# Optimization experiments

Hardware: AMD Instinct MI355X
Metric: run time of the kernel (lower is better)

Reference implementation:

```python
import jax, jax.numpy as jnp
import numpy as np

NUM_STEPS = 32
SEQ = 64
IN = 512
HID = 256
NUM_CLASSES = 10
BATCH = 2048


def _lstm_layer(xseq, Wih, Whh, bih, bhh):
    # xseq: (T, B, D). PyTorch LSTMCell gate order: i, f, g, o.
    B = xseq.shape[1]
    H = Whh.shape[1]
    h0 = jnp.zeros((B, H), xseq.dtype)
    c0 = jnp.zeros((B, H), xseq.dtype)
    b = bih + bhh

    def step(carry, x):
        h, c = carry
        gates = x @ Wih.T + h @ Whh.T + b  # (B, 4H)
        i, f, g, o = jnp.split(gates, 4, axis=-1)
        c_new = jax.nn.sigmoid(f) * c + jax.nn.sigmoid(i) * jnp.tanh(g)
        h_new = jax.nn.sigmoid(o) * jnp.tanh(c_new)
        return (h_new, c_new), h_new

    (hT, cT), hs = jax.lax.scan(step, (h0, c0), xseq)
    return hs, hT


def _run_stack(xseq, layer_params):
    hT = None
    for (Wih, Whh, bih, bhh) in layer_params:
        xseq, hT = _lstm_layer(xseq, Wih, Whh, bih, bhh)
    return hT


def setup_inputs() -> dict:
    key = jax.random.key(0)
    ks = jax.random.split(key, 32)
    d = {"xs": jax.random.normal(ks[0], (BATCH, SEQ, IN), dtype=jnp.float32)}
    cfg = [IN, HID, HID]
    ki = 1
    for direc in ("f", "r"):
        for l, (di, dh) in enumerate(zip(cfg[:-1], cfg[1:])):
            s = 1.0 / np.sqrt(dh)
            d[f"Wih_{direc}{l}"] = jax.random.uniform(ks[ki], (4 * dh, di), minval=-s, maxval=s); ki += 1
            d[f"Whh_{direc}{l}"] = jax.random.uniform(ks[ki], (4 * dh, dh), minval=-s, maxval=s); ki += 1
            d[f"bih_{direc}{l}"] = jax.random.uniform(ks[ki], (4 * dh,), minval=-s, maxval=s); ki += 1
            d[f"bhh_{direc}{l}"] = jax.random.uniform(ks[ki], (4 * dh,), minval=-s, maxval=s); ki += 1
    s = 1.0 / np.sqrt(2 * HID)
    d["W3"] = jax.random.uniform(ks[ki], (NUM_CLASSES, 2 * HID), minval=-s, maxval=s); ki += 1
    d["b3"] = jax.random.uniform(ks[ki], (NUM_CLASSES,), minval=-s, maxval=s)
    return d


def reference(xs, Wih_f0, Whh_f0, bih_f0, bhh_f0, Wih_f1, Whh_f1, bih_f1, bhh_f1,
              Wih_r0, Whh_r0, bih_r0, bhh_r0, Wih_r1, Whh_r1, bih_r1, bhh_r1, W3, b3):
    # forward direction: timesteps 62-NUM_STEPS .. 61
    xf = jnp.transpose(xs[:, 62 - NUM_STEPS:62, :], (1, 0, 2))  # (T, B, D)
    hF = _run_stack(xf, [(Wih_f0, Whh_f0, bih_f0, bhh_f0),
                         (Wih_f1, Whh_f1, bih_f1, bhh_f1)])
    # reverse direction: last 3 frames in order 63, 62, 61
    xr = jnp.transpose(jnp.flip(xs[:, 61:64, :], axis=1), (1, 0, 2))  # (3, B, D)
    hR = _run_stack(xr, [(Wih_r0, Whh_r0, bih_r0, bhh_r0),
                         (Wih_r1, Whh_r1, bih_r1, bhh_r1)])
    latent = jnp.concatenate([hF, hR], axis=1)  # (B, 512)
    return latent @ W3.T + b3
```

## Files before the change

kernel.cpp:

```cpp
#include <hip/hip_runtime.h>
#include <stdint.h>

typedef unsigned short u16;
typedef unsigned long long u64;
typedef __attribute__((ext_vector_type(8)))  short  bf16x8;
typedef __attribute__((ext_vector_type(8)))  u16    u16x8;
typedef __attribute__((ext_vector_type(4)))  float  f32x4;
typedef __attribute__((ext_vector_type(16))) _Float16 f16x16;

#define MFMA_BF16(a,b,c) __builtin_amdgcn_mfma_f32_16x16x32_bf16((a),(b),(c),0,0,0)

#define BATCH   2048
#define FSTEPS  32
#define RSTEPS  3
#define NVF     35

static constexpr size_t HROW32 = 128;
static constexpr size_t HPAR32 = (size_t)BATCH * HROW32;

static constexpr size_t OFF_CTL  = 0;
static constexpr size_t OFF_H0G  = 32768;
static constexpr size_t OFF_H1G  = OFF_H0G + HPAR32 * 2 * 4;
static constexpr size_t OFF_LAT  = OFF_H1G + HPAR32 * 2 * 4;
static constexpr size_t OFF_XP   = OFF_LAT + (size_t)BATCH * 512 * 4;
static constexpr size_t XP_BYTES = (size_t)NVF * BATCH * 1024 * 2;
static constexpr size_t OFF_W0XF = OFF_XP + XP_BYTES;
static constexpr size_t OFF_W0XR = OFF_W0XF + (size_t)1024 * 512 * 2;
static constexpr size_t OFF_P0F  = OFF_W0XR + (size_t)1024 * 512 * 2;
static constexpr size_t OFF_P0R  = OFF_P0F + (size_t)32768 * 16;
static constexpr size_t OFF_P1F  = OFF_P0R + (size_t)32768 * 16;
static constexpr size_t OFF_P1R  = OFF_P1F + (size_t)65536 * 16;
static constexpr size_t OFF_BS0F = OFF_P1R + (size_t)65536 * 16;
static constexpr size_t OFF_BS0R = OFF_BS0F + 4096;
static constexpr size_t OFF_BS1F = OFF_BS0R + 4096;
static constexpr size_t OFF_BS1R = OFF_BS1F + 4096;
static constexpr size_t WS_NEED  = OFF_BS1R + 4096;

__device__ __forceinline__ u16 f2bf(float f) {
    unsigned u = __float_as_uint(f);
    unsigned r = (u + 0x7fffu + ((u >> 16) & 1u)) >> 16;
    return (u16)r;
}
__device__ __forceinline__ float sigm(float x) { return 1.0f / (1.0f + __expf(-x)); }
__device__ __forceinline__ float tanh_fast(float x) {
    float a = fabsf(x);
    float e = __expf(-2.0f * a);
    float t = (1.0f - e) / (1.0f + e);
    return x < 0.0f ? -t : t;
}

__device__ __forceinline__ bf16x8 ldsA(const char* H, int row, int k) {
    int byte = (row << 9) + (k << 1);
    byte ^= (row & 7) << 4;
    return *(const bf16x8*)(H + byte);
}

__device__ __forceinline__ void reload32(char* Hs, const u64* src, int rg, int tid) {
    u64 v[8];
#pragma unroll
    for (int i = 0; i < 8; ++i) {
        int idx = tid + (i << 8);
        v[i] = __hip_atomic_load(src + ((size_t)rg * 32 + (idx >> 6)) * 64 + (idx & 63),
                                 __ATOMIC_RELAXED, __HIP_MEMORY_SCOPE_AGENT);
    }
#pragma unroll
    for (int i = 0; i < 8; ++i) {
        int idx = tid + (i << 8);
        int row = idx >> 6, cu = idx & 63;
        int byte = (row << 9) + (cu << 3);
        byte ^= (row & 7) << 4;
        *(u64*)(Hs + byte) = v[i];
    }
}

__global__ void __launch_bounds__(256)
lstm_seq(const _Float16* __restrict__ xp,
         const u16* __restrict__ P0f_, const u16* __restrict__ P0r_,
         const u16* __restrict__ P1f_, const u16* __restrict__ P1r_,
         const float* __restrict__ bs1f, const float* __restrict__ bs1r,
         unsigned* __restrict__ h0g, unsigned* __restrict__ h1g,
         float* __restrict__ latent, unsigned* __restrict__ ctl)
{
    __shared__ char T0[16384];
    __shared__ char T1[16384];
    const int tid = threadIdx.x, wq = tid >> 6, lane = tid & 63;
    const int bid = blockIdx.x;
    const int colq = bid >> 6;
    const int rg   = bid & 63;
    const int mem  = colq * 4 + wq;
    const int hc   = mem * 16 + (lane & 15);
    const int klane = lane >> 4, q4 = klane << 2;
    unsigned* flag = ctl + (size_t)rg * 64;
    unsigned bcount = 0;

    for (int dir = 0; dir < 2; ++dir) {
        const int nst = dir ? RSTEPS : FSTEPS;
        const int gbase = dir ? FSTEPS : 0;
        const bf16x8* P0v = (const bf16x8*)(dir ? P0r_ : P0f_) + (size_t)mem * (8 * 4 * 64);
        const bf16x8* P1v = (const bf16x8*)(dir ? P1r_ : P1f_) + (size_t)mem * (16 * 4 * 64);
        const float* bs1 = dir ? bs1r : bs1f;
        float b1reg[4];
#pragma unroll
        for (int g = 0; g < 4; ++g) b1reg[g] = bs1[g * 256 + hc];

        float c0[2][4], c1[2][4];
#pragma unroll
        for (int Mt = 0; Mt < 2; ++Mt)
#pragma unroll
            for (int r = 0; r < 4; ++r) { c0[Mt][r] = 0.f; c1[Mt][r] = 0.f; }

        __syncthreads();
#pragma unroll
        for (int i = 0; i < 4; ++i) {
            ((f32x4*)T0)[i * 256 + tid] = (f32x4){0.f, 0.f, 0.f, 0.f};
            ((f32x4*)T1)[i * 256 + tid] = (f32x4){0.f, 0.f, 0.f, 0.f};
        }
        __syncthreads();

        f16x16 xqm[2];
#pragma unroll
        for (int Mt = 0; Mt < 2; ++Mt)
            xqm[Mt] = *(const f16x16*)(xp +
                ((((size_t)gbase * 128 + rg * 2 + Mt) * 16 + mem) * 64 + lane) * 16);

        for (int t = 0; t <= nst; ++t) {
            f32x4 acc1[4][2];
            if (t >= 1) {
#pragma unroll
                for (int g = 0; g < 4; ++g) { acc1[g][0] = (f32x4){0.f,0.f,0.f,0.f}; acc1[g][1] = (f32x4){0.f,0.f,0.f,0.f}; }
#pragma unroll
                for (int kc = 0; kc < 8; ++kc) {
                    bf16x8 a0 = ldsA(T0, (lane & 15),       kc * 32 + klane * 8);
                    bf16x8 a1 = ldsA(T0, 16 + (lane & 15),  kc * 32 + klane * 8);
#pragma unroll
                    for (int g = 0; g < 4; ++g) {
                        bf16x8 b = P1v[(kc * 4 + g) * 64 + lane];
                        acc1[g][0] = MFMA_BF16(a0, b, acc1[g][0]);
                        acc1[g][1] = MFMA_BF16(a1, b, acc1[g][1]);
                    }
                }
                if (t >= 2) {
#pragma unroll
                    for (int kc = 0; kc < 8; ++kc) {
                        bf16x8 a0 = ldsA(T1, (lane & 15),      kc * 32 + klane * 8);
                        bf16x8 a1 = ldsA(T1, 16 + (lane & 15), kc * 32 + klane * 8);
#pragma unroll
                        for (int g = 0; g < 4; ++g) {
                            bf16x8 b = P1v[((kc + 8) * 4 + g) * 64 + lane];
                            acc1[g][0] = MFMA_BF16(a0, b, acc1[g][0]);
                            acc1[g][1] = MFMA_BF16(a1, b, acc1[g][1]);
                        }
                    }
                }
            }

            f32x4 acc0[4][2];
            if (t < nst) {
#pragma unroll
                for (int g = 0; g < 4; ++g) { acc0[g][0] = (f32x4){0.f,0.f,0.f,0.f}; acc0[g][1] = (f32x4){0.f,0.f,0.f,0.f}; }
                if (t >= 1) {
#pragma unroll
                    for (int kc = 0; kc < 8; ++kc) {
                        bf16x8 a0 = ldsA(T0, (lane & 15),      kc * 32 + klane * 8);
                        bf16x8 a1 = ldsA(T0, 16 + (lane & 15), kc * 32 + klane * 8);
#pragma unroll
                        for (int g = 0; g < 4; ++g) {
                            bf16x8 b = P0v[(kc * 4 + g) * 64 + lane];
                            acc0[g][0] = MFMA_BF16(a0, b, acc0[g][0]);
                            acc0[g][1] = MFMA_BF16(a1, b, acc0[g][1]);
                        }
                    }
                }
            }

            if (t < nst) {
                unsigned* dst = h0g + (size_t)(t & 1) * HPAR32;
                const int cp = mem * 8 + ((lane & 15) >> 1);
#pragma unroll
                for (int Mt = 0; Mt < 2; ++Mt) {
                    float hn[4];
#pragma unroll
                    for (int r = 0; r < 4; ++r) {
                        float gi = acc0[0][Mt][r] + (float)xqm[Mt][0 * 4 + r];
                        float gf = acc0[1][Mt][r] + (float)xqm[Mt][1 * 4 + r];
                        float gg = acc0[2][Mt][r] + (float)xqm[Mt][2 * 4 + r];
                        float go = acc0[3][Mt][r] + (float)xqm[Mt][3 * 4 + r];
                        float cn = sigm(gf) * c0[Mt][r] + sigm(gi) * tanh_fast(gg);
                        c0[Mt][r] = cn;
                        hn[r] = sigm(go) * tanh_fast(cn);
                    }
                    const int rowbase = rg * 32 + Mt * 16 + q4;
#pragma unroll
                    for (int r = 0; r < 4; ++r) {
                        float p = __shfl_xor(hn[r], 1);
                        if (!(lane & 1)) {
                            unsigned w = (unsigned)f2bf(hn[r]) | ((unsigned)f2bf(p) << 16);
                            __hip_atomic_store(dst + (size_t)(rowbase + r) * HROW32 + cp, w,
                                               __ATOMIC_RELAXED, __HIP_MEMORY_SCOPE_AGENT);
                        }
                    }
                }
            }

            if (t >= 1) {
                const int cp = mem * 8 + ((lane & 15) >> 1);
#pragma unroll
                for (int Mt = 0; Mt < 2; ++Mt) {
                    float hn[4];
#pragma unroll
                    for (int r = 0; r < 4; ++r) {
                        float gi = acc1[0][Mt][r] + b1reg[0];
                        float gf = acc1[1][Mt][r] + b1reg[1];
                        float gg = acc1[2][Mt][r] + b1reg[2];
                        float go = acc1[3][Mt][r] + b1reg[3];
                        float cn = sigm(gf) * c1[Mt][r] + sigm(gi) * tanh_fast(gg);
                        c1[Mt][r] = cn;
                        hn[r] = sigm(go) * tanh_fast(cn);
                    }
                    const int rowbase = rg * 32 + Mt * 16 + q4;
                    if (t < nst) {
                        unsigned* dst = h1g + (size_t)((t - 1) & 1) * HPAR32;
#pragma unroll
                        for (int r = 0; r < 4; ++r) {
                            float p = __shfl_xor(hn[r], 1);
                            if (!(lane & 1)) {
                                unsigned w = (unsigned)f2bf(hn[r]) | ((unsigned)f2bf(p) << 16);
                                __hip_atomic_store(dst + (size_t)(rowbase + r) * HROW32 + cp, w,
                                                   __ATOMIC_RELAXED, __HIP_MEMORY_SCOPE_AGENT);
                            }
                        }
                    } else {
#pragma unroll
                        for (int r = 0; r < 4; ++r)
                            latent[(size_t)(rowbase + r) * 512 + dir * 256 + hc] = hn[r];
                    }
                }
            }

            if (t < nst) {
                ++bcount;
                asm volatile("s_waitcnt vmcnt(0)" ::: "memory");
                __syncthreads();
                if (tid == 0)
                    __hip_atomic_fetch_add(flag, 1u, __ATOMIC_RELAXED, __HIP_MEMORY_SCOPE_AGENT);
                if (t + 1 < nst) {
#pragma unroll
                    for (int Mt = 0; Mt < 2; ++Mt)
                        xqm[Mt] = *(const f16x16*)(xp +
                            ((((size_t)(gbase + t + 1) * 128 + rg * 2 + Mt) * 16 + mem) * 64 + lane) * 16);
                }
                if (tid == 0) {
                    while (__hip_atomic_load(flag, __ATOMIC_RELAXED, __HIP_MEMORY_SCOPE_AGENT)
                           < 4u * bcount) {}
                }
                __syncthreads();
                __builtin_amdgcn_sched_barrier(0);
                reload32(T0, (const u64*)(h0g + (size_t)(t & 1) * HPAR32), rg, tid);
                if (t >= 1)
                    reload32(T1, (const u64*)(h1g + (size_t)((t - 1) & 1) * HPAR32), rg, tid);
                __syncthreads();
            }
        }
    }
}

__global__ void __launch_bounds__(256)
xproj_gemm(const float* __restrict__ xs,
           const u16* __restrict__ W0xf, const u16* __restrict__ W0xr,
           const float* __restrict__ bs0f, const float* __restrict__ bs0r,
           _Float16* __restrict__ xp)
{
    __shared__ char As[16384];
    __shared__ char Bs[16384];
    const int tid = threadIdx.x, wv = tid >> 6, lane = tid & 63;
    const int phys = blockIdx.x;
    const int xcd = phys & 7, idx = phys >> 3;
    const int mt = xcd * 70 + (idx >> 3);
    const int nt = idx & 7;
    const int vf = mt >> 4;
    const int dirr = (vf >= 32);
    const int frame = dirr ? (95 - vf) : (30 + vf);
    const int brow = (mt & 15) * 128;
    const u16* Wp = (dirr ? W0xr : W0xf) + (size_t)nt * 128 * 512;
    const float* bs = dirr ? bs0r : bs0f;

    float breg[8];
#pragma unroll
    for (int n = 0; n < 8; ++n) breg[n] = bs[nt * 128 + n * 16 + (lane & 15)];

    f32x4 acc[8][2];
#pragma unroll
    for (int n = 0; n < 8; ++n) { acc[n][0] = (f32x4){0.f,0.f,0.f,0.f}; acc[n][1] = (f32x4){0.f,0.f,0.f,0.f}; }

    const int ar = tid >> 1, akoff = (tid & 1) * 32;
    const float* asrc0 = xs + ((size_t)(brow + ar) * 64 + frame) * 512 + akoff;

    for (int c = 0; c < 8; ++c) {
        {
            const float* s = asrc0 + c * 64;
            u16x8 o[4];
#pragma unroll
            for (int j2 = 0; j2 < 4; ++j2) {
                float4 f0 = *(const float4*)(s + j2 * 8);
                float4 f1 = *(const float4*)(s + j2 * 8 + 4);
                u16x8 o_;
                o_[0] = f2bf(f0.x); o_[1] = f2bf(f0.y); o_[2] = f2bf(f0.z); o_[3] = f2bf(f0.w);
                o_[4] = f2bf(f1.x); o_[5] = f2bf(f1.y); o_[6] = f2bf(f1.z); o_[7] = f2bf(f1.w);
                o[j2] = o_;
            }
#pragma unroll
            for (int j2 = 0; j2 < 4; ++j2) {
                int k = akoff + j2 * 8;
                int byte = (ar << 7) + (k << 1); byte ^= (ar & 7) << 4;
                *(u16x8*)(As + byte) = o[j2];
            }
        }
#pragma unroll
        for (int i = 0; i < 4; ++i) {
            int u = tid + i * 256;
            int ns = u >> 3, c8 = (u & 7) << 3;
            u16x8 v = *(const u16x8*)(Wp + (size_t)ns * 512 + c * 64 + c8);
            int byte = (ns << 7) + (c8 << 1); byte ^= (ns & 7) << 4;
            *(u16x8*)(Bs + byte) = v;
        }
        __syncthreads();
#pragma unroll
        for (int kk = 0; kk < 2; ++kk) {
            int kin = kk * 32 + (lane >> 4) * 8;
            bf16x8 a0, a1;
            int row = wv * 32 + (lane & 15);
            int byte = (row << 7) + (kin << 1); byte ^= (row & 7) << 4;
            a0 = *(const bf16x8*)(As + byte);
            int row1 = row + 16;
            byte = (row1 << 7) + (kin << 1); byte ^= (row1 & 7) << 4;
            a1 = *(const bf16x8*)(As + byte);
#pragma unroll
            for (int n = 0; n < 8; ++n) {
                int ns = n * 16 + (lane & 15);
                int bb = (ns << 7) + (kin << 1); bb ^= (ns & 7) << 4;
                bf16x8 bf_ = *(const bf16x8*)(Bs + bb);
                acc[n][0] = MFMA_BF16(a0, bf_, acc[n][0]);
                acc[n][1] = MFMA_BF16(a1, bf_, acc[n][1]);
            }
        }
        __syncthreads();
    }
#pragma unroll
    for (int n = 0; n < 8; ++n)
#pragma unroll
        for (int mm = 0; mm < 2; ++mm)
#pragma unroll
            for (int r = 0; r < 4; ++r) {
                int vm  = mt * 128 + wv * 32 + mm * 16 + ((lane >> 4) << 2) + r;
                int col = nt * 128 + n * 16 + (lane & 15);
                int vf2 = vm >> 11, brow2 = vm & 2047;
                int rb2 = brow2 >> 4, sub = brow2 & 15;
                int lane2 = ((sub >> 2) << 4) + (col & 15);
                int m2 = (col >> 4) & 15, g2 = col >> 8;
                size_t o = ((((size_t)vf2 * 128 + rb2) * 16 + m2) * 64 + lane2) * 16
                           + (g2 << 2) + (sub & 3);
                xp[o] = (_Float16)(acc[n][mm][r] + breg[n]);
            }
}

__global__ void pack_w(const float* __restrict__ Wa, int da,
                       const float* __restrict__ bi, const float* __restrict__ bh,
                       u16* __restrict__ Wout, float* __restrict__ bout)
{
    int total = 1024 * da;
    int gt = blockIdx.x * blockDim.x + threadIdx.x;
    int stride = gridDim.x * blockDim.x;
    for (int i = gt; i < total; i += stride) Wout[i] = f2bf(Wa[i]);
    if (bout && gt < 1024) bout[gt] = bi[gt] + bh[gt];
}

__global__ void pack_frag(const float* __restrict__ Wa, int da,
                          const float* __restrict__ Wb, int db,
                          int nkc, u16* __restrict__ out,
                          const float* __restrict__ bi, const float* __restrict__ bh,
                          float* __restrict__ bout)
{
    int total = 16 * nkc * 4 * 64;
    int gt = blockIdx.x * blockDim.x + threadIdx.x;
    int stride = gridDim.x * blockDim.x;
    for (int u = gt; u < total; u += stride) {
        int l = u & 63;
        int t1 = u >> 6;
        int g = t1 & 3;
        int t2 = t1 >> 2;
        int kc = t2 % nkc;
        int mem = t2 / nkc;
        int row = g * 256 + mem * 16 + (l & 15);
        int k0 = kc * 32 + ((l >> 4) << 3);
        u16x8 o;
#pragma unroll
        for (int jj = 0; jj < 8; ++jj) {
            int k = k0 + jj;
            float v = (k < da) ? Wa[(size_t)row * da + k] : Wb[(size_t)row * db + (k - da)];
            o[jj] = f2bf(v);
        }
        *(u16x8*)(out + (size_t)u * 8) = o;
    }
    if (bout && gt < 1024) bout[gt] = bi[gt] + bh[gt];
}

__global__ void final_linear(const float* __restrict__ latent, const float* __restrict__ W3,
                             const float* __restrict__ b3, float* __restrict__ out)
{
    int idx = blockIdx.x * blockDim.x + threadIdx.x;
    if (idx >= BATCH * 10) return;
    int bb = idx / 10, c = idx - bb * 10;
    const float* lrow = latent + (size_t)bb * 512;
    const float* wrow = W3 + (size_t)c * 512;
    float s = b3[c];
#pragma unroll 4
    for (int k = 0; k < 512; k += 4) {
        float4 lv = *(const float4*)(lrow + k);
        float4 wv = *(const float4*)(wrow + k);
        s += lv.x * wv.x + lv.y * wv.y + lv.z * wv.z + lv.w * wv.w;
    }
    out[idx] = s;
}

extern "C" void kernel_launch(void* const* d_in, const int* in_sizes, int n_in,
                              void* d_out, int out_size, void* d_ws, size_t ws_size,
                              hipStream_t stream)
{
    (void)in_sizes; (void)n_in; (void)out_size;
    if (ws_size < WS_NEED) return;

    const float* xs     = (const float*)d_in[0];
    const float* Wih_f0 = (const float*)d_in[1];
    const float* Whh_f0 = (const float*)d_in[2];
    const float* bih_f0 = (const float*)d_in[3];
    const float* bhh_f0 = (const float*)d_in[4];
    const float* Wih_f1 = (const float*)d_in[5];
    const float* Whh_f1 = (const float*)d_in[6];
    const float* bih_f1 = (const float*)d_in[7];
    const float* bhh_f1 = (const float*)d_in[8];
    const float* Wih_r0 = (const float*)d_in[9];
    const float* Whh_r0 = (const float*)d_in[10];
    const float* bih_r0 = (const float*)d_in[11];
    const float* bhh_r0 = (const float*)d_in[12];
    const float* Wih_r1 = (const float*)d_in[13];
    const float* Whh_r1 = (const float*)d_in[14];
    const float* bih_r1 = (const float*)d_in[15];
    const float* bhh_r1 = (const float*)d_in[16];
    const float* W3     = (const float*)d_in[17];
    const float* b3     = (const float*)d_in[18];

    char* ws = (char*)d_ws;
    unsigned* ctl = (unsigned*)(ws + OFF_CTL);
    unsigned* h0g = (unsigned*)(ws + OFF_H0G);
    unsigned* h1g = (unsigned*)(ws + OFF_H1G);
    float* latent = (float*)(ws + OFF_LAT);
    _Float16* xp  = (_Float16*)(ws + OFF_XP);
    u16* W0xf = (u16*)(ws + OFF_W0XF);
    u16* W0xr = (u16*)(ws + OFF_W0XR);
    u16* P0f  = (u16*)(ws + OFF_P0F);
    u16* P0r  = (u16*)(ws + OFF_P0R);
    u16* P1f  = (u16*)(ws + OFF_P1F);
    u16* P1r  = (u16*)(ws + OFF_P1R);
    float* bs0f = (float*)(ws + OFF_BS0F);
    float* bs0r = (float*)(ws + OFF_BS0R);
    float* bs1f = (float*)(ws + OFF_BS1F);
    float* bs1r = (float*)(ws + OFF_BS1R);

    hipMemsetAsync(ctl, 0, 32768, stream);

    pack_w<<<256, 256, 0, stream>>>(Wih_f0, 512, bih_f0, bhh_f0, W0xf, bs0f);
    pack_w<<<256, 256, 0, stream>>>(Wih_r0, 512, bih_r0, bhh_r0, W0xr, bs0r);
    pack_frag<<<64, 256, 0, stream>>>(Whh_f0, 256, Whh_f0, 0, 8,  P0f, nullptr, nullptr, nullptr);
    pack_frag<<<64, 256, 0, stream>>>(Whh_r0, 256, Whh_r0, 0, 8,  P0r, nullptr, nullptr, nullptr);
    pack_frag<<<64, 256, 0, stream>>>(Wih_f1, 256, Whh_f1, 256, 16, P1f, bih_f1, bhh_f1, bs1f);
    pack_frag<<<64, 256, 0, stream>>>(Wih_r1, 256, Whh_r1, 256, 16, P1r, bih_r1, bhh_r1, bs1r);

    xproj_gemm<<<4480, 256, 0, stream>>>(xs, W0xf, W0xr, bs0f, bs0r, xp);

    lstm_seq<<<256, 256, 0, stream>>>(xp, P0f, P0r, P1f, P1r, bs1f, bs1r,
                                      h0g, h1g, latent, ctl);

    final_linear<<<80, 256, 0, stream>>>(latent, W3, b3, (float*)d_out);
}
```

Before: 871.1 us.

## Split recurrent LSTM matmuls across two wave groups and pre-convert inputs to bf16

The persistent LSTM kernel now runs 512 threads per block. Two halves of the waves split the layer-0 and layer-1 recurrent K work, exchange partial accumulators through LDS, and each half applies one layer's gate nonlinearity. The aim is to shorten the serial per-step critical path by using more waves per CU. A separate pack_x kernel converts the needed input frames to bf16 once, so the projection GEMM can load bf16 directly instead of converting fp32 per tile. This adds an extra LDS round trip and sync per step, plus an extra pass over the input.

```diff
diff --git a/kernel.cpp b/kernel.cpp
--- a/kernel.cpp
+++ b/kernel.cpp
@@ -14,27 +14,10 @@
 #define FSTEPS  32
 #define RSTEPS  3
 #define NVF     35
+#define NXF     34
 
 static constexpr size_t HROW32 = 128;
 static constexpr size_t HPAR32 = (size_t)BATCH * HROW32;
-
-static constexpr size_t OFF_CTL  = 0;
-static constexpr size_t OFF_H0G  = 32768;
-static constexpr size_t OFF_H1G  = OFF_H0G + HPAR32 * 2 * 4;
-static constexpr size_t OFF_LAT  = OFF_H1G + HPAR32 * 2 * 4;
-static constexpr size_t OFF_XP   = OFF_LAT + (size_t)BATCH * 512 * 4;
-static constexpr size_t XP_BYTES = (size_t)NVF * BATCH * 1024 * 2;
-static constexpr size_t OFF_W0XF = OFF_XP + XP_BYTES;
-static constexpr size_t OFF_W0XR = OFF_W0XF + (size_t)1024 * 512 * 2;
-static constexpr size_t OFF_P0F  = OFF_W0XR + (size_t)1024 * 512 * 2;
-static constexpr size_t OFF_P0R  = OFF_P0F + (size_t)32768 * 16;
-static constexpr size_t OFF_P1F  = OFF_P0R + (size_t)32768 * 16;
-static constexpr size_t OFF_P1R  = OFF_P1F + (size_t)65536 * 16;
-static constexpr size_t OFF_BS0F = OFF_P1R + (size_t)65536 * 16;
-static constexpr size_t OFF_BS0R = OFF_BS0F + 4096;
-static constexpr size_t OFF_BS1F = OFF_BS0R + 4096;
-static constexpr size_t OFF_BS1R = OFF_BS1F + 4096;
-static constexpr size_t WS_NEED  = OFF_BS1R + 4096;
 
 __device__ __forceinline__ u16 f2bf(float f) {
     unsigned u = __float_as_uint(f);
@@ -55,17 +38,17 @@
     return *(const bf16x8*)(H + byte);
 }
 
-__device__ __forceinline__ void reload32(char* Hs, const u64* src, int rg, int tid) {
-    u64 v[8];
-#pragma unroll
-    for (int i = 0; i < 8; ++i) {
-        int idx = tid + (i << 8);
+__device__ __forceinline__ void reload512(char* Hs, const u64* src, int rg, int tid) {
+    u64 v[4];
+#pragma unroll
+    for (int i = 0; i < 4; ++i) {
+        int idx = tid + (i << 9);
         v[i] = __hip_atomic_load(src + ((size_t)rg * 32 + (idx >> 6)) * 64 + (idx & 63),
                                  __ATOMIC_RELAXED, __HIP_MEMORY_SCOPE_AGENT);
     }
 #pragma unroll
-    for (int i = 0; i < 8; ++i) {
-        int idx = tid + (i << 8);
+    for (int i = 0; i < 4; ++i) {
+        int idx = tid + (i << 9);
         int row = idx >> 6, cu = idx & 63;
         int byte = (row << 9) + (cu << 3);
         byte ^= (row & 7) << 4;
@@ -73,7 +56,7 @@
     }
 }
 
-__global__ void __launch_bounds__(256)
+__global__ void __launch_bounds__(512, 1)
 lstm_seq(const _Float16* __restrict__ xp,
          const u16* __restrict__ P0f_, const u16* __restrict__ P0r_,
          const u16* __restrict__ P1f_, const u16* __restrict__ P1r_,
@@ -81,15 +64,21 @@
          unsigned* __restrict__ h0g, unsigned* __restrict__ h1g,
          float* __restrict__ latent, unsigned* __restrict__ ctl)
 {
-    __shared__ char T0[16384];
-    __shared__ char T1[16384];
-    const int tid = threadIdx.x, wq = tid >> 6, lane = tid & 63;
+    extern __shared__ char lds[];
+    char* T0 = lds;
+    char* T1 = lds + 16384;
+    char* SA = lds + 32768;
+    char* SB = lds + 65536;
+
+    const int tid = threadIdx.x, w = tid >> 6, lane = tid & 63;
+    const int wq = w & 3, kh = w >> 2;
     const int bid = blockIdx.x;
     const int colq = bid >> 6;
     const int rg   = bid & 63;
     const int mem  = colq * 4 + wq;
     const int hc   = mem * 16 + (lane & 15);
     const int klane = lane >> 4, q4 = klane << 2;
+    const int sbase = (wq * 64 + lane) * 16;
     unsigned* flag = ctl + (size_t)rg * 64;
     unsigned bcount = 0;
 
@@ -111,34 +100,56 @@
 
         __syncthreads();
 #pragma unroll
-        for (int i = 0; i < 4; ++i) {
-            ((f32x4*)T0)[i * 256 + tid] = (f32x4){0.f, 0.f, 0.f, 0.f};
-            ((f32x4*)T1)[i * 256 + tid] = (f32x4){0.f, 0.f, 0.f, 0.f};
+        for (int i = 0; i < 4; ++i)
+            ((f32x4*)lds)[i * 512 + tid] = (f32x4){0.f, 0.f, 0.f, 0.f};
+        __syncthreads();
+
+        f16x16 xqm[2];
+        if (kh == 1) {
+#pragma unroll
+            for (int Mt = 0; Mt < 2; ++Mt)
+                xqm[Mt] = *(const f16x16*)(xp +
+                    ((((size_t)gbase * 128 + rg * 2 + Mt) * 16 + mem) * 64 + lane) * 16);
         }
-        __syncthreads();
-
-        f16x16 xqm[2];
-#pragma unroll
-        for (int Mt = 0; Mt < 2; ++Mt)
-            xqm[Mt] = *(const f16x16*)(xp +
-                ((((size_t)gbase * 128 + rg * 2 + Mt) * 16 + mem) * 64 + lane) * 16);
 
         for (int t = 0; t <= nst; ++t) {
-            f32x4 acc1[4][2];
-            if (t >= 1) {
-#pragma unroll
-                for (int g = 0; g < 4; ++g) { acc1[g][0] = (f32x4){0.f,0.f,0.f,0.f}; acc1[g][1] = (f32x4){0.f,0.f,0.f,0.f}; }
-#pragma unroll
-                for (int kc = 0; kc < 8; ++kc) {
-                    bf16x8 a0 = ldsA(T0, (lane & 15),       kc * 32 + klane * 8);
-                    bf16x8 a1 = ldsA(T0, 16 + (lane & 15),  kc * 32 + klane * 8);
-#pragma unroll
-                    for (int g = 0; g < 4; ++g) {
-                        bf16x8 b = P1v[(kc * 4 + g) * 64 + lane];
-                        acc1[g][0] = MFMA_BF16(a0, b, acc1[g][0]);
-                        acc1[g][1] = MFMA_BF16(a1, b, acc1[g][1]);
+            f32x4 acc1[4][2], acc0[4][2];
+#pragma unroll
+            for (int g = 0; g < 4; ++g)
+#pragma unroll
+                for (int Mt = 0; Mt < 2; ++Mt) {
+                    acc1[g][Mt] = (f32x4){0.f, 0.f, 0.f, 0.f};
+                    acc0[g][Mt] = (f32x4){0.f, 0.f, 0.f, 0.f};
+                }
+
+            if (kh == 0) {
+                if (t >= 1) {
+#pragma unroll
+                    for (int kc = 0; kc < 8; ++kc) {
+                        bf16x8 a0 = ldsA(T0, (lane & 15),      kc * 32 + klane * 8);
+                        bf16x8 a1 = ldsA(T0, 16 + (lane & 15), kc * 32 + klane * 8);
+#pragma unroll
+                        for (int g = 0; g < 4; ++g) {
+                            bf16x8 b = P1v[(kc * 4 + g) * 64 + lane];
+                            acc1[g][0] = MFMA_BF16(a0, b, acc1[g][0]);
+                            acc1[g][1] = MFMA_BF16(a1, b, acc1[g][1]);
+                        }
                     }
-                }
+                    if (t < nst) {
+#pragma unroll
+                        for (int kc = 0; kc < 4; ++kc) {
+                            bf16x8 a0 = ldsA(T0, (lane & 15),      kc * 32 + klane * 8);
+                            bf16x8 a1 = ldsA(T0, 16 + (lane & 15), kc * 32 + klane * 8);
+#pragma unroll
+                            for (int g = 0; g < 4; ++g) {
+                                bf16x8 b = P0v[(kc * 4 + g) * 64 + lane];
+                                acc0[g][0] = MFMA_BF16(a0, b, acc0[g][0]);
+                                acc0[g][1] = MFMA_BF16(a1, b, acc0[g][1]);
+                            }
+                        }
+                    }
+                }
+            } else {
                 if (t >= 2) {
 #pragma unroll
                     for (int kc = 0; kc < 8; ++kc) {
@@ -152,15 +163,9 @@
                         }
                     }
                 }
-            }
-
-            f32x4 acc0[4][2];
-            if (t < nst) {
-#pragma unroll
-                for (int g = 0; g < 4; ++g) { acc0[g][0] = (f32x4){0.f,0.f,0.f,0.f}; acc0[g][1] = (f32x4){0.f,0.f,0.f,0.f}; }
-                if (t >= 1) {
-#pragma unroll
-                    for (int kc = 0; kc < 8; ++kc) {
+                if (t >= 1 && t < nst) {
+#pragma unroll
+                    for (int kc = 4; kc < 8; ++kc) {
                         bf16x8 a0 = ldsA(T0, (lane & 15),      kc * 32 + klane * 8);
                         bf16x8 a1 = ldsA(T0, 16 + (lane & 15), kc * 32 + klane * 8);
 #pragma unroll
@@ -173,66 +178,89 @@
                 }
             }
 
-            if (t < nst) {
-                unsigned* dst = h0g + (size_t)(t & 1) * HPAR32;
-                const int cp = mem * 8 + ((lane & 15) >> 1);
-#pragma unroll
-                for (int Mt = 0; Mt < 2; ++Mt) {
-                    float hn[4];
-#pragma unroll
-                    for (int r = 0; r < 4; ++r) {
-                        float gi = acc0[0][Mt][r] + (float)xqm[Mt][0 * 4 + r];
-                        float gf = acc0[1][Mt][r] + (float)xqm[Mt][1 * 4 + r];
-                        float gg = acc0[2][Mt][r] + (float)xqm[Mt][2 * 4 + r];
-                        float go = acc0[3][Mt][r] + (float)xqm[Mt][3 * 4 + r];
-                        float cn = sigm(gf) * c0[Mt][r] + sigm(gi) * tanh_fast(gg);
-                        c0[Mt][r] = cn;
-                        hn[r] = sigm(go) * tanh_fast(cn);
+            {
+                char* S = kh ? SA : SB;
+#pragma unroll
+                for (int g = 0; g < 4; ++g)
+#pragma unroll
+                    for (int Mt = 0; Mt < 2; ++Mt)
+                        *(f32x4*)(S + (g * 2 + Mt) * 4096 + sbase) =
+                            kh ? acc1[g][Mt] : acc0[g][Mt];
+            }
+            __syncthreads();
+
+            if (kh == 0) {
+                if (t >= 1) {
+#pragma unroll
+                    for (int g = 0; g < 4; ++g)
+#pragma unroll
+                        for (int Mt = 0; Mt < 2; ++Mt)
+                            acc1[g][Mt] += *(const f32x4*)(SA + (g * 2 + Mt) * 4096 + sbase);
+                    const int cp = mem * 8 + ((lane & 15) >> 1);
+#pragma unroll
+                    for (int Mt = 0; Mt < 2; ++Mt) {
+                        float hn[4];
+#pragma unroll
+                        for (int r = 0; r < 4; ++r) {
+                            float gi = acc1[0][Mt][r] + b1reg[0];
+                            float gf = acc1[1][Mt][r] + b1reg[1];
+                            float gg = acc1[2][Mt][r] + b1reg[2];
+                            float go = acc1[3][Mt][r] + b1reg[3];
+                            float cn = sigm(gf) * c1[Mt][r] + sigm(gi) * tanh_fast(gg);
+                            c1[Mt][r] = cn;
+                            hn[r] = sigm(go) * tanh_fast(cn);
+                        }
+                        const int rowbase = rg * 32 + Mt * 16 + q4;
+                        if (t < nst) {
+                            unsigned* dst = h1g + (size_t)((t - 1) & 1) * HPAR32;
+#pragma unroll
+                            for (int r = 0; r < 4; ++r) {
+                                float p = __shfl_xor(hn[r], 1);
+                                if (!(lane & 1)) {
+                                    unsigned wv_ = (unsigned)f2bf(hn[r]) | ((unsigned)f2bf(p) << 16);
+                                    __hip_atomic_store(dst + (size_t)(rowbase + r) * HROW32 + cp, wv_,
+                                                       __ATOMIC_RELAXED, __HIP_MEMORY_SCOPE_AGENT);
+                                }
+                            }
+                        } else {
+#pragma unroll
+                            for (int r = 0; r < 4; ++r)
+                                latent[(size_t)(rowbase + r) * 512 + dir * 256 + hc] = hn[r];
+                        }
                     }
-                    const int rowbase = rg * 32 + Mt * 16 + q4;
-#pragma unroll
-                    for (int r = 0; r < 4; ++r) {
-                        float p = __shfl_xor(hn[r], 1);
-                        if (!(lane & 1)) {
-                            unsigned w = (unsigned)f2bf(hn[r]) | ((unsigned)f2bf(p) << 16);
-                            __hip_atomic_store(dst + (size_t)(rowbase + r) * HROW32 + cp, w,
-                                               __ATOMIC_RELAXED, __HIP_MEMORY_SCOPE_AGENT);
-                        }
-                    }
-                }
-            }
-
-            if (t >= 1) {
-                const int cp = mem * 8 + ((lane & 15) >> 1);
-#pragma unroll
-                for (int Mt = 0; Mt < 2; ++Mt) {
-                    float hn[4];
-#pragma unroll
-                    for (int r = 0; r < 4; ++r) {
-                        float gi = acc1[0][Mt][r] + b1reg[0];
-                        float gf = acc1[1][Mt][r] + b1reg[1];
-                        float gg = acc1[2][Mt][r] + b1reg[2];
-                        float go = acc1[3][Mt][r] + b1reg[3];
-                        float cn = sigm(gf) * c1[Mt][r] + sigm(gi) * tanh_fast(gg);
-                        c1[Mt][r] = cn;
-                        hn[r] = sigm(go) * tanh_fast(cn);
-                    }
-                    const int rowbase = rg * 32 + Mt * 16 + q4;
-                    if (t < nst) {
-                        unsigned* dst = h1g + (size_t)((t - 1) & 1) * HPAR32;
+                }
+            } else {
+                if (t < nst) {
+#pragma unroll
+                    for (int g = 0; g < 4; ++g)
+#pragma unroll
+                        for (int Mt = 0; Mt < 2; ++Mt)
+                            acc0[g][Mt] += *(const f32x4*)(SB + (g * 2 + Mt) * 4096 + sbase);
+                    unsigned* dst = h0g + (size_t)(t & 1) * HPAR32;
+                    const int cp = mem * 8 + ((lane & 15) >> 1);
+#pragma unroll
+                    for (int Mt = 0; Mt < 2; ++Mt) {
+                        float hn[4];
+#pragma unroll
+                        for (int r = 0; r < 4; ++r) {
+                            float gi = acc0[0][Mt][r] + (float)xqm[Mt][0 * 4 + r];
+                            float gf = acc0[1][Mt][r] + (float)xqm[Mt][1 * 4 + r];
+                            float gg = acc0[2][Mt][r] + (float)xqm[Mt][2 * 4 + r];
+                            float go = acc0[3][Mt][r] + (float)xqm[Mt][3 * 4 + r];
+                            float cn = sigm(gf) * c0[Mt][r] + sigm(gi) * tanh_fast(gg);
+                            c0[Mt][r] = cn;
+                            hn[r] = sigm(go) * tanh_fast(cn);
+                        }
+                        const int rowbase = rg * 32 + Mt * 16 + q4;
 #pragma unroll
                         for (int r = 0; r < 4; ++r) {
                             float p = __shfl_xor(hn[r], 1);
                             if (!(lane & 1)) {
-                                unsigned w = (unsigned)f2bf(hn[r]) | ((unsigned)f2bf(p) << 16);
-                                __hip_atomic_store(dst + (size_t)(rowbase + r) * HROW32 + cp, w,
+                                unsigned wv_ = (unsigned)f2bf(hn[r]) | ((unsigned)f2bf(p) << 16);
+                                __hip_atomic_store(dst + (size_t)(rowbase + r) * HROW32 + cp, wv_,
                                                    __ATOMIC_RELAXED, __HIP_MEMORY_SCOPE_AGENT);
                             }
                         }
-                    } else {
-#pragma unroll
-                        for (int r = 0; r < 4; ++r)
-                            latent[(size_t)(rowbase + r) * 512 + dir * 256 + hc] = hn[r];
                     }
                 }
             }
@@ -243,7 +271,7 @@
                 __syncthreads();
                 if (tid == 0)
                     __hip_atomic_fetch_add(flag, 1u, __ATOMIC_RELAXED, __HIP_MEMORY_SCOPE_AGENT);
-                if (t + 1 < nst) {
+                if (kh == 1 && t + 1 < nst) {
 #pragma unroll
                     for (int Mt = 0; Mt < 2; ++Mt)
                         xqm[Mt] = *(const f16x16*)(xp +
@@ -255,17 +283,18 @@
                 }
                 __syncthreads();
                 __builtin_amdgcn_sched_barrier(0);
-                reload32(T0, (const u64*)(h0g + (size_t)(t & 1) * HPAR32), rg, tid);
+                reload512(T0, (const u64*)(h0g + (size_t)(t & 1) * HPAR32), rg, tid);
                 if (t >= 1)
-                    reload32(T1, (const u64*)(h1g + (size_t)((t - 1) & 1) * HPAR32), rg, tid);
+                    reload512(T1, (const u64*)(h1g + (size_t)((t - 1) & 1) * HPAR32), rg, tid);
                 __syncthreads();
             }
         }
     }
 }
 
+template<bool PRE>
 __global__ void __launch_bounds__(256)
-xproj_gemm(const float* __restrict__ xs,
+xproj_gemm(const float* __restrict__ xs, const u16* __restrict__ xbf,
            const u16* __restrict__ W0xf, const u16* __restrict__ W0xr,
            const float* __restrict__ bs0f, const float* __restrict__ bs0r,
            _Float16* __restrict__ xp)
@@ -293,11 +322,23 @@
     for (int n = 0; n < 8; ++n) { acc[n][0] = (f32x4){0.f,0.f,0.f,0.f}; acc[n][1] = (f32x4){0.f,0.f,0.f,0.f}; }
 
     const int ar = tid >> 1, akoff = (tid & 1) * 32;
-    const float* asrc0 = xs + ((size_t)(brow + ar) * 64 + frame) * 512 + akoff;
+    const float* asrcf = xs + ((size_t)(brow + ar) * 64 + frame) * 512 + akoff;
+    const u16*   asrcb = xbf + (((size_t)(frame - 30) * 2048 + brow + ar) * 512 + akoff);
 
     for (int c = 0; c < 8; ++c) {
-        {
-            const float* s = asrc0 + c * 64;
+        if constexpr (PRE) {
+            u16x8 o[4];
+#pragma unroll
+            for (int j2 = 0; j2 < 4; ++j2)
+                o[j2] = *(const u16x8*)(asrcb + c * 64 + j2 * 8);
+#pragma unroll
+            for (int j2 = 0; j2 < 4; ++j2) {
+                int k = akoff + j2 * 8;
+                int byte = (ar << 7) + (k << 1); byte ^= (ar & 7) << 4;
+                *(u16x8*)(As + byte) = o[j2];
+            }
+        } else {
+            const float* s = asrcf + c * 64;
             u16x8 o[4];
 #pragma unroll
             for (int j2 = 0; j2 < 4; ++j2) {
@@ -372,6 +413,24 @@
     int stride = gridDim.x * blockDim.x;
     for (int i = gt; i < total; i += stride) Wout[i] = f2bf(Wa[i]);
     if (bout && gt < 1024) bout[gt] = bi[gt] + bh[gt];
+}
+
+__global__ void pack_x(const float* __restrict__ xs, u16* __restrict__ xbf)
+{
+    const size_t total = (size_t)NXF * BATCH * 512 / 8;
+    for (size_t u = (size_t)blockIdx.x * blockDim.x + threadIdx.x; u < total;
+         u += (size_t)gridDim.x * blockDim.x) {
+        size_t k8 = (u & 63) << 3;
+        size_t bb = (u >> 6) & (BATCH - 1);
+        size_t f  = u >> 17;
+        const float* s = xs + (bb * 64 + 30 + f) * 512 + k8;
+        float4 v0 = *(const float4*)s;
+        float4 v1 = *(const float4*)(s + 4);
+        u16x8 o;
+        o[0] = f2bf(v0.x); o[1] = f2bf(v0.y); o[2] = f2bf(v0.z); o[3] = f2bf(v0.w);
+        o[4] = f2bf(v1.x); o[5] = f2bf(v1.y); o[6] = f2bf(v1.z); o[7] = f2bf(v1.w);
+        *(u16x8*)(xbf + ((f * BATCH + bb) * 512 + k8)) = o;
+    }
 }
 
 __global__ void pack_frag(const float* __restrict__ Wa, int da,
@@ -427,7 +486,6 @@
                               hipStream_t stream)
 {
     (void)in_sizes; (void)n_in; (void)out_size;
-    if (ws_size < WS_NEED) return;
 
     const float* xs     = (const float*)d_in[0];
     const float* Wih_f0 = (const float*)d_in[1];
@@ -449,22 +507,54 @@
     const float* W3     = (const float*)d_in[17];
     const float* b3     = (const float*)d_in[18];
 
+    const size_t XP_BYTES  = (size_t)NVF * BATCH * 1024 * 2;
+    const size_t XBF_BYTES = (size_t)NXF * BATCH * 512 * 2;
+    auto layout = [&](bool with_xbf, size_t* off) {
+        size_t o = 0;
+        off[0] = o; o += 32768;
+        off[1] = o; o += HPAR32 * 2 * 4;
+        off[2] = o; o += HPAR32 * 2 * 4;
+        off[3] = o; o += (size_t)BATCH * 512 * 4;
+        off[4] = o; o += XP_BYTES;
+        off[5] = o; o += (size_t)1024 * 512 * 2;
+        off[6] = o; o += (size_t)1024 * 512 * 2;
+        off[7] = o; o += (size_t)32768 * 16;
+        off[8] = o; o += (size_t)32768 * 16;
+        off[9] = o; o += (size_t)65536 * 16;
+        off[10] = o; o += (size_t)65536 * 16;
+        off[11] = o; o += 4096;
+        off[12] = o; o += 4096;
+        off[13] = o; o += 4096;
+        off[14] = o; o += 4096;
+        off[15] = o; o += with_xbf ? XBF_BYTES : 0;
+        return o;
+    };
+    size_t off[16];
+    bool pre = true;
+    size_t need = layout(true, off);
+    if (ws_size < need) {
+        pre = false;
+        need = layout(false, off);
+        if (ws_size < need) return;
+    }
+
     char* ws = (char*)d_ws;
-    unsigned* ctl = (unsigned*)(ws + OFF_CTL);
-    unsigned* h0g = (unsigned*)(ws + OFF_H0G);
-    unsigned* h1g = (unsigned*)(ws + OFF_H1G);
-    float* latent = (float*)(ws + OFF_LAT);
-    _Float16* xp  = (_Float16*)(ws + OFF_XP);
-    u16* W0xf = (u16*)(ws + OFF_W0XF);
-    u16* W0xr = (u16*)(ws + OFF_W0XR);
-    u16* P0f  = (u16*)(ws + OFF_P0F);
-    u16* P0r  = (u16*)(ws + OFF_P0R);
-    u16* P1f  = (u16*)(ws + OFF_P1F);
-    u16* P1r  = (u16*)(ws + OFF_P1R);
-    float* bs0f = (float*)(ws + OFF_BS0F);
-    float* bs0r = (float*)(ws + OFF_BS0R);
-    float* bs1f = (float*)(ws + OFF_BS1F);
-    float* bs1r = (float*)(ws + OFF_BS1R);
+    unsigned* ctl = (unsigned*)(ws + off[0]);
+    unsigned* h0g = (unsigned*)(ws + off[1]);
+    unsigned* h1g = (unsigned*)(ws + off[2]);
+    float* latent = (float*)(ws + off[3]);
+    _Float16* xp  = (_Float16*)(ws + off[4]);
+    u16* W0xf = (u16*)(ws + off[5]);
+    u16* W0xr = (u16*)(ws + off[6]);
+    u16* P0f  = (u16*)(ws + off[7]);
+    u16* P0r  = (u16*)(ws + off[8]);
+    u16* P1f  = (u16*)(ws + off[9]);
+    u16* P1r  = (u16*)(ws + off[10]);
+    float* bs0f = (float*)(ws + off[11]);
+    float* bs0r = (float*)(ws + off[12]);
+    float* bs1f = (float*)(ws + off[13]);
+    float* bs1r = (float*)(ws + off[14]);
+    u16* xbf  = (u16*)(ws + off[15]);
 
     hipMemsetAsync(ctl, 0, 32768, stream);
 
@@ -475,10 +565,17 @@
     pack_frag<<<64, 256, 0, stream>>>(Wih_f1, 256, Whh_f1, 256, 16, P1f, bih_f1, bhh_f1, bs1f);
     pack_frag<<<64, 256, 0, stream>>>(Wih_r1, 256, Whh_r1, 256, 16, P1r, bih_r1, bhh_r1, bs1r);
 
-    xproj_gemm<<<4480, 256, 0, stream>>>(xs, W0xf, W0xr, bs0f, bs0r, xp);
-
-    lstm_seq<<<256, 256, 0, stream>>>(xp, P0f, P0r, P1f, P1r, bs1f, bs1r,
-                                      h0g, h1g, latent, ctl);
+    if (pre) {
+        pack_x<<<2048, 256, 0, stream>>>(xs, xbf);
+        xproj_gemm<true><<<4480, 256, 0, stream>>>(xs, xbf, W0xf, W0xr, bs0f, bs0r, xp);
+    } else {
+        xproj_gemm<false><<<4480, 256, 0, stream>>>(xs, xbf, W0xf, W0xr, bs0f, bs0r, xp);
+    }
+
+    hipFuncSetAttribute((const void*)lstm_seq,
+                        hipFuncAttributeMaxDynamicSharedMemorySize, 98304);
+    lstm_seq<<<256, 512, 98304, stream>>>(xp, P0f, P0r, P1f, P1r, bs1f, bs1r,
+                                          h0g, h1g, latent, ctl);
 
     final_linear<<<80, 256, 0, stream>>>(latent, W3, b3, (float*)d_out);
 }
```

Measured after the change: 1.033 ms. 1.19x slower.

## Split LSTM recurrence across 512 blocks with one M-tile per wave

Applied to the files above, without the earlier changes.

The recurrent kernel now launches 512 blocks instead of 256. Each wave handles a single 16-row M-tile for one column member, where before each wave covered two M-tiles. Blocks are remapped so that 8 blocks share a row group, and the per-row-group barrier now waits for 8 arrivals instead of 4. The aim is to halve per-wave MFMA and gate work per timestep and spread the recurrence over more CUs, at the cost of reloading the weight fragments twice and synchronising more blocks in each grid-wide step barrier.

```diff
diff --git a/kernel.cpp b/kernel.cpp
--- a/kernel.cpp
+++ b/kernel.cpp
@@ -83,13 +83,16 @@
 {
     __shared__ char T0[16384];
     __shared__ char T1[16384];
-    const int tid = threadIdx.x, wq = tid >> 6, lane = tid & 63;
+    const int tid = threadIdx.x, w = tid >> 6, lane = tid & 63;
+    const int ms = w & 1, Mt = w >> 1;
     const int bid = blockIdx.x;
-    const int colq = bid >> 6;
-    const int rg   = bid & 63;
-    const int mem  = colq * 4 + wq;
-    const int hc   = mem * 16 + (lane & 15);
+    const int xq_ = bid & 7, qq = bid >> 3;
+    const int rg  = xq_ * 8 + (qq >> 3);
+    const int cg  = qq & 7;
+    const int mem = cg * 2 + ms;
+    const int hc  = mem * 16 + (lane & 15);
     const int klane = lane >> 4, q4 = klane << 2;
+    const int arow = Mt * 16 + (lane & 15);
     unsigned* flag = ctl + (size_t)rg * 64;
     unsigned bcount = 0;
 
@@ -103,11 +106,9 @@
 #pragma unroll
         for (int g = 0; g < 4; ++g) b1reg[g] = bs1[g * 256 + hc];
 
-        float c0[2][4], c1[2][4];
-#pragma unroll
-        for (int Mt = 0; Mt < 2; ++Mt)
-#pragma unroll
-            for (int r = 0; r < 4; ++r) { c0[Mt][r] = 0.f; c1[Mt][r] = 0.f; }
+        float c0[4], c1[4];
+#pragma unroll
+        for (int r = 0; r < 4; ++r) { c0[r] = 0.f; c1[r] = 0.f; }
 
         __syncthreads();
 #pragma unroll
@@ -117,58 +118,43 @@
         }
         __syncthreads();
 
-        f16x16 xqm[2];
-#pragma unroll
-        for (int Mt = 0; Mt < 2; ++Mt)
-            xqm[Mt] = *(const f16x16*)(xp +
-                ((((size_t)gbase * 128 + rg * 2 + Mt) * 16 + mem) * 64 + lane) * 16);
+        f16x16 xqm = *(const f16x16*)(xp +
+            ((((size_t)gbase * 128 + rg * 2 + Mt) * 16 + mem) * 64 + lane) * 16);
 
         for (int t = 0; t <= nst; ++t) {
-            f32x4 acc1[4][2];
+            f32x4 acc1[4];
             if (t >= 1) {
 #pragma unroll
-                for (int g = 0; g < 4; ++g) { acc1[g][0] = (f32x4){0.f,0.f,0.f,0.f}; acc1[g][1] = (f32x4){0.f,0.f,0.f,0.f}; }
+                for (int g = 0; g < 4; ++g) acc1[g] = (f32x4){0.f, 0.f, 0.f, 0.f};
 #pragma unroll
                 for (int kc = 0; kc < 8; ++kc) {
-                    bf16x8 a0 = ldsA(T0, (lane & 15),       kc * 32 + klane * 8);
-                    bf16x8 a1 = ldsA(T0, 16 + (lane & 15),  kc * 32 + klane * 8);
-#pragma unroll
-                    for (int g = 0; g < 4; ++g) {
-                        bf16x8 b = P1v[(kc * 4 + g) * 64 + lane];
-                        acc1[g][0] = MFMA_BF16(a0, b, acc1[g][0]);
-                        acc1[g][1] = MFMA_BF16(a1, b, acc1[g][1]);
+                    bf16x8 a = ldsA(T0, arow, kc * 32 + klane * 8);
+#pragma unroll
+                    for (int g = 0; g < 4; ++g)
+                        acc1[g] = MFMA_BF16(a, P1v[(kc * 4 + g) * 64 + lane], acc1[g]);
+                }
+                if (t >= 2) {
+#pragma unroll
+                    for (int kc = 0; kc < 8; ++kc) {
+                        bf16x8 a = ldsA(T1, arow, kc * 32 + klane * 8);
+#pragma unroll
+                        for (int g = 0; g < 4; ++g)
+                            acc1[g] = MFMA_BF16(a, P1v[((kc + 8) * 4 + g) * 64 + lane], acc1[g]);
                     }
                 }
-                if (t >= 2) {
+            }
+
+            f32x4 acc0[4];
+            if (t < nst) {
+#pragma unroll
+                for (int g = 0; g < 4; ++g) acc0[g] = (f32x4){0.f, 0.f, 0.f, 0.f};
+                if (t >= 1) {
 #pragma unroll
                     for (int kc = 0; kc < 8; ++kc) {
-                        bf16x8 a0 = ldsA(T1, (lane & 15),      kc * 32 + klane * 8);
-                        bf16x8 a1 = ldsA(T1, 16 + (lane & 15), kc * 32 + klane * 8);
-#pragma unroll
-                        for (int g = 0; g < 4; ++g) {
-                            bf16x8 b = P1v[((kc + 8) * 4 + g) * 64 + lane];
-                            acc1[g][0] = MFMA_BF16(a0, b, acc1[g][0]);
-                            acc1[g][1] = MFMA_BF16(a1, b, acc1[g][1]);
-                        }
-                    }
-                }
-            }
-
-            f32x4 acc0[4][2];
-            if (t < nst) {
-#pragma unroll
-                for (int g = 0; g < 4; ++g) { acc0[g][0] = (f32x4){0.f,0.f,0.f,0.f}; acc0[g][1] = (f32x4){0.f,0.f,0.f,0.f}; }
-                if (t >= 1) {
-#pragma unroll
-                    for (int kc = 0; kc < 8; ++kc) {
-                        bf16x8 a0 = ldsA(T0, (lane & 15),      kc * 32 + klane * 8);
-                        bf16x8 a1 = ldsA(T0, 16 + (lane & 15), kc * 32 + klane * 8);
-#pragma unroll
-                        for (int g = 0; g < 4; ++g) {
-                            bf16x8 b = P0v[(kc * 4 + g) * 64 + lane];
-                            acc0[g][0] = MFMA_BF16(a0, b, acc0[g][0]);
-                            acc0[g][1] = MFMA_BF16(a1, b, acc0[g][1]);
-                        }
+                        bf16x8 a = ldsA(T0, arow, kc * 32 + klane * 8);
+#pragma unroll
+                        for (int g = 0; g < 4; ++g)
+                            acc0[g] = MFMA_BF16(a, P0v[(kc * 4 + g) * 64 + lane], acc0[g]);
                     }
                 }
             }
@@ -176,64 +162,58 @@
             if (t < nst) {
                 unsigned* dst = h0g + (size_t)(t & 1) * HPAR32;
                 const int cp = mem * 8 + ((lane & 15) >> 1);
-#pragma unroll
-                for (int Mt = 0; Mt < 2; ++Mt) {
-                    float hn[4];
-#pragma unroll
-                    for (int r = 0; r < 4; ++r) {
-                        float gi = acc0[0][Mt][r] + (float)xqm[Mt][0 * 4 + r];
-                        float gf = acc0[1][Mt][r] + (float)xqm[Mt][1 * 4 + r];
-                        float gg = acc0[2][Mt][r] + (float)xqm[Mt][2 * 4 + r];
-                        float go = acc0[3][Mt][r] + (float)xqm[Mt][3 * 4 + r];
-                        float cn = sigm(gf) * c0[Mt][r] + sigm(gi) * tanh_fast(gg);
-                        c0[Mt][r] = cn;
-                        hn[r] = sigm(go) * tanh_fast(cn);
+                float hn[4];
+#pragma unroll
+                for (int r = 0; r < 4; ++r) {
+                    float gi = acc0[0][r] + (float)xqm[0 * 4 + r];
+                    float gf = acc0[1][r] + (float)xqm[1 * 4 + r];
+                    float gg = acc0[2][r] + (float)xqm[2 * 4 + r];
+                    float go = acc0[3][r] + (float)xqm[3 * 4 + r];
+                    float cn = sigm(gf) * c0[r] + sigm(gi) * tanh_fast(gg);
+                    c0[r] = cn;
+                    hn[r] = sigm(go) * tanh_fast(cn);
+                }
+                const int rowbase = rg * 32 + Mt * 16 + q4;
+#pragma unroll
+                for (int r = 0; r < 4; ++r) {
+                    float p = __shfl_xor(hn[r], 1);
+                    if (!(lane & 1)) {
+                        unsigned wv_ = (unsigned)f2bf(hn[r]) | ((unsigned)f2bf(p) << 16);
+                        __hip_atomic_store(dst + (size_t)(rowbase + r) * HROW32 + cp, wv_,
+                                           __ATOMIC_RELAXED, __HIP_MEMORY_SCOPE_AGENT);
                     }
-                    const int rowbase = rg * 32 + Mt * 16 + q4;
+                }
+            }
+
+            if (t >= 1) {
+                const int cp = mem * 8 + ((lane & 15) >> 1);
+                float hn[4];
+#pragma unroll
+                for (int r = 0; r < 4; ++r) {
+                    float gi = acc1[0][r] + b1reg[0];
+                    float gf = acc1[1][r] + b1reg[1];
+                    float gg = acc1[2][r] + b1reg[2];
+                    float go = acc1[3][r] + b1reg[3];
+                    float cn = sigm(gf) * c1[r] + sigm(gi) * tanh_fast(gg);
+                    c1[r] = cn;
+                    hn[r] = sigm(go) * tanh_fast(cn);
+                }
+                const int rowbase = rg * 32 + Mt * 16 + q4;
+                if (t < nst) {
+                    unsigned* dst = h1g + (size_t)((t - 1) & 1) * HPAR32;
 #pragma unroll
                     for (int r = 0; r < 4; ++r) {
                         float p = __shfl_xor(hn[r], 1);
                         if (!(lane & 1)) {
-                            unsigned w = (unsigned)f2bf(hn[r]) | ((unsigned)f2bf(p) << 16);
-                            __hip_atomic_store(dst + (size_t)(rowbase + r) * HROW32 + cp, w,
+                            unsigned wv_ = (unsigned)f2bf(hn[r]) | ((unsigned)f2bf(p) << 16);
+                            __hip_atomic_store(dst + (size_t)(rowbase + r) * HROW32 + cp, wv_,
                                                __ATOMIC_RELAXED, __HIP_MEMORY_SCOPE_AGENT);
                         }
                     }
-                }
-            }
-
-            if (t >= 1) {
-                const int cp = mem * 8 + ((lane & 15) >> 1);
-#pragma unroll
-                for (int Mt = 0; Mt < 2; ++Mt) {
-                    float hn[4];
-#pragma unroll
-                    for (int r = 0; r < 4; ++r) {
-                        float gi = acc1[0][Mt][r] + b1reg[0];
-                        float gf = acc1[1][Mt][r] + b1reg[1];
-                        float gg = acc1[2][Mt][r] + b1reg[2];
-                        float go = acc1[3][Mt][r] + b1reg[3];
-                        float cn = sigm(gf) * c1[Mt][r] + sigm(gi) * tanh_fast(gg);
-                        c1[Mt][r] = cn;
-                        hn[r] = sigm(go) * tanh_fast(cn);
-                    }
-                    const int rowbase = rg * 32 + Mt * 16 + q4;
-                    if (t < nst) {
-                        unsigned* dst = h1g + (size_t)((t - 1) & 1) * HPAR32;
-#pragma unroll
-                        for (int r = 0; r < 4; ++r) {
-                            float p = __shfl_xor(hn[r], 1);
-                            if (!(lane & 1)) {
-                                unsigned w = (unsigned)f2bf(hn[r]) | ((unsigned)f2bf(p) << 16);
-                                __hip_atomic_store(dst + (size_t)(rowbase + r) * HROW32 + cp, w,
-                                                   __ATOMIC_RELAXED, __HIP_MEMORY_SCOPE_AGENT);
-                            }
-                        }
-                    } else {
-#pragma unroll
-                        for (int r = 0; r < 4; ++r)
-                            latent[(size_t)(rowbase + r) * 512 + dir * 256 + hc] = hn[r];
-                    }
+                } else {
+#pragma unroll
+                    for (int r = 0; r < 4; ++r)
+                        latent[(size_t)(rowbase + r) * 512 + dir * 256 + hc] = hn[r];
                 }
             }
 
@@ -244,14 +224,12 @@
                 if (tid == 0)
                     __hip_atomic_fetch_add(flag, 1u, __ATOMIC_RELAXED, __HIP_MEMORY_SCOPE_AGENT);
                 if (t + 1 < nst) {
-#pragma unroll
-                    for (int Mt = 0; Mt < 2; ++Mt)
-                        xqm[Mt] = *(const f16x16*)(xp +
-                            ((((size_t)(gbase + t + 1) * 128 + rg * 2 + Mt) * 16 + mem) * 64 + lane) * 16);
+                    xqm = *(const f16x16*)(xp +
+                        ((((size_t)(gbase + t + 1) * 128 + rg * 2 + Mt) * 16 + mem) * 64 + lane) * 16);
                 }
                 if (tid == 0) {
                     while (__hip_atomic_load(flag, __ATOMIC_RELAXED, __HIP_MEMORY_SCOPE_AGENT)
-                           < 4u * bcount) {}
+                           < 8u * bcount) {}
                 }
                 __syncthreads();
                 __builtin_amdgcn_sched_barrier(0);
@@ -477,7 +455,7 @@
 
     xproj_gemm<<<4480, 256, 0, stream>>>(xs, W0xf, W0xr, bs0f, bs0r, xp);
 
-    lstm_seq<<<256, 256, 0, stream>>>(xp, P0f, P0r, P1f, P1r, bs1f, bs1r,
+    lstm_seq<<<512, 256, 0, stream>>>(xp, P0f, P0r, P1f, P1r, bs1f, bs1r,
                                       h0g, h1g, latent, ctl);
 
     final_linear<<<80, 256, 0, stream>>>(latent, W3, b3, (float*)d_out);
```

Result: slower. 1.215 ms (+39.5%).
